# Performance work log

Hardware: AMD Instinct MI355X
Metric: run time of the kernel (lower is better)

Reference implementation:

```python
import jax, jax.numpy as jnp
import numpy as np

B, U, N, D, O = 64, 8, 2048, 512, 512  # batch, units, neurons, input_dim, output_dim
RES_CONN, IN_CONN, BIAS_P = 0.2, 0.2, 0.5


def setup_inputs() -> dict:
    key = jax.random.key(0)
    ks = jax.random.split(key, 10)
    # Recurrent weights: normal * sparse mask, normalized by ~spectral radius
    Wd = jax.random.normal(ks[0], (U, N, N), dtype=jnp.float32)
    Wmask = (jax.random.uniform(ks[1], (U, N, N)) < RES_CONN).astype(jnp.float32)
    W = Wd * Wmask / jnp.sqrt(RES_CONN * N)  # approx unit spectral radius
    # Input weights: fixed_bernoulli -> {0,1} sparse matrix
    Win = (jax.random.uniform(ks[2], (U, D, N)) < IN_CONN).astype(jnp.float32)
    bias = (jax.random.uniform(ks[3], (U, 1, N)) < BIAS_P).astype(jnp.float32)
    Wout = jax.random.normal(ks[4], (U, N, O), dtype=jnp.float32)
    sr = jax.random.uniform(ks[5], (U, 1, 1), dtype=jnp.float32)
    adaptive_lr = jax.random.uniform(ks[6], (U, D, 1), dtype=jnp.float32)
    temperature = jnp.ones((1,), dtype=jnp.float32)
    X = jax.random.normal(ks[7], (B, U, D), dtype=jnp.float32)
    state = jax.random.normal(ks[8], (B, U, N), dtype=jnp.float32)
    return {"X": X, "state": state, "W": W, "Win": Win, "bias": bias,
            "Wout": Wout, "sr": sr, "adaptive_lr": adaptive_lr,
            "temperature": temperature}


def reference(X, state, W, Win, bias, Wout, sr, adaptive_lr, temperature):
    # X: [B,U,D], state: [B,U,N]
    x = X[:, :, None, :]       # [B,U,1,D]
    s = state[:, :, None, :]   # [B,U,1,N]
    # adaptive learning rate: softmax over units
    logits = jnp.einsum('buid,udk->buik', x, adaptive_lr) / temperature  # [B,U,1,1]
    lr = jax.nn.softmax(logits, axis=1)
    # _sparse_mm_subhead == masked matmul (W's zeros contribute nothing)
    feed = jnp.einsum('bud,udn->bun', X, Win)[:, :, None, :]           # [B,U,1,N]
    echo = jnp.einsum('bun,unm->bum', state, W * sr)[:, :, None, :] + bias
    new_state = (1.0 - lr) * s + lr * jnp.tanh(feed + echo)            # [B,U,1,N]
    output = jnp.einsum('buin,uno->buio', new_state, Wout)             # [B,U,1,O]
    return new_state.squeeze(2), output.squeeze(2)
```

## Files before the change

### kernel.cpp

```cpp
#include <hip/hip_runtime.h>

#define B_ 64
#define U_ 8
#define N_ 2048
#define D_ 512
#define O_ 512
#define NS_ELEMS ((long)B_ * U_ * N_)
#define OUT_ELEMS ((long)B_ * U_ * O_)

typedef __attribute__((ext_vector_type(8))) short short8;
typedef __attribute__((ext_vector_type(8))) float float8;
typedef __attribute__((ext_vector_type(4))) float float4v;
typedef __attribute__((ext_vector_type(4))) unsigned short ushort4v;
typedef __attribute__((ext_vector_type(16))) float floatx16;

__device__ __forceinline__ float bf2f(unsigned short b) {
    unsigned int u = ((unsigned int)b) << 16;
    float f; __builtin_memcpy(&f, &u, 4); return f;
}
__device__ __forceinline__ unsigned short f2bf(float f) {
    unsigned int u; __builtin_memcpy(&u, &f, 4);
    u += 0x7FFFu + ((u >> 16) & 1u);
    return (unsigned short)(u >> 16);
}
__device__ __forceinline__ bool is_bf(const void* temp) {
    return ((const unsigned short*)temp)[0] == 0x3F80u;
}
__device__ __forceinline__ float ldg1(const void* p, long i, bool bf) {
    return bf ? bf2f(((const unsigned short*)p)[i]) : ((const float*)p)[i];
}
__device__ __forceinline__ short8 ld8(const void* p, long i, bool bf) {
    if (bf) return *(const short8*)((const unsigned short*)p + i);
    float8 v = *(const float8*)((const float*)p + i);
    short8 r;
#pragma unroll
    for (int e = 0; e < 8; ++e) r[e] = (short)f2bf(v[e]);
    return r;
}
__device__ __forceinline__ short8 ld8s(const void* p, long i, bool bf, float s) {
    short8 r;
    if (bf) {
        short8 v = *(const short8*)((const unsigned short*)p + i);
#pragma unroll
        for (int e = 0; e < 8; ++e) r[e] = (short)f2bf(bf2f((unsigned short)v[e]) * s);
    } else {
        float8 v = *(const float8*)((const float*)p + i);
#pragma unroll
        for (int e = 0; e < 8; ++e) r[e] = (short)f2bf(v[e] * s);
    }
    return r;
}
__device__ __forceinline__ void stg1(void* p, long i, bool bf, float v) {
    if (bf) ((unsigned short*)p)[i] = f2bf(v); else ((float*)p)[i] = v;
}
__device__ __forceinline__ int swz(int row, int kbyte) {
    return row * 128 + (kbyte ^ ((row & 7) << 4));
}

__device__ __forceinline__ void gl_lds16(const void* g, void* l) {
    __builtin_amdgcn_global_load_lds(
        (const __attribute__((address_space(1))) unsigned int*)g,
        (__attribute__((address_space(3))) unsigned int*)l, 16, 0, 0);
}
#define WAITV(n) asm volatile("s_waitcnt vmcnt(" #n ")" ::: "memory")

template<bool BF, int NCH>
__device__ __forceinline__ void gemm_wide(
        const char* __restrict__ Apan, long arow_b,
        const char* __restrict__ Bpan, long brow_b,
        char* __restrict__ As,
        char* __restrict__ Bs,
        floatx16& acc0, floatx16& acc1, int t) {
    const int w = t >> 6, l = t & 63;
    const int mrow = (w >> 1) * 32 + (l & 31);
    const int nc0 = (w & 1) * 64 + (l & 31);
    const int BCH = BF ? 16384 : 32768;
    const int a_r = w * 16 + (l >> 3);
    const long a_g = 16 * ((l & 7) ^ (l >> 3));

#define ISSUE2(ck)                                                                  \
    {   char* Ad = As + ((ck) & 1) * 8192 + w * 2048;                               \
        const char* Ag0 = Apan + (long)(ck) * 128;                                  \
        gl_lds16(Ag0 + (long)a_r * arow_b + a_g, Ad);                               \
        gl_lds16(Ag0 + (long)(a_r + 8) * arow_b + a_g, Ad + 1024);                  \
        char* Bd = Bs + ((ck) & 1) * BCH;                                           \
        if (BF) {                                                                   \
            _Pragma("unroll")                                                       \
            for (int i = 0; i < 4; ++i) {                                           \
                int kr = (ck) * 64 + w * 16 + i * 4 + (l >> 4);                     \
                gl_lds16(Bpan + (long)kr * brow_b + (l & 15) * 16,                  \
                         Bd + (w * 16 + i * 4) * 256);                              \
            }                                                                       \
        } else {                                                                    \
            _Pragma("unroll")                                                       \
            for (int i = 0; i < 8; ++i) {                                           \
                int kr = (ck) * 64 + w * 16 + i * 2 + (l >> 5);                     \
                gl_lds16(Bpan + (long)kr * brow_b + (l & 31) * 16,                  \
                         Bd + (w * 16 + i * 2) * 512);                              \
            }                                                                       \
        } }

    ISSUE2(0);
#pragma unroll
    for (int ck = 0; ck < NCH; ++ck) {
        if (ck + 1 < NCH) ISSUE2(ck + 1);
        __builtin_amdgcn_sched_barrier(0);
        if (ck + 1 < NCH) { if (BF) { WAITV(6); } else { WAITV(10); } }
        else { WAITV(0); }
        __builtin_amdgcn_s_barrier();
        __builtin_amdgcn_sched_barrier(0);
        const char* Ac = As + (ck & 1) * 8192;
        const char* Bc = Bs + (ck & 1) * BCH;
#pragma unroll
        for (int ks = 0; ks < 4; ++ks) {
            int g = 2 * ks + (l >> 5);
            short8 a = *(const short8*)(Ac + swz(mrow, g * 16));
            short8 b0, b1;
            if (BF) {
#pragma unroll
                for (int e = 0; e < 8; ++e) {
                    b0[e] = *(const short*)(Bc + (g * 8 + e) * 256 + nc0 * 2);
                    b1[e] = *(const short*)(Bc + (g * 8 + e) * 256 + (nc0 + 32) * 2);
                }
            } else {
#pragma unroll
                for (int e = 0; e < 8; ++e) {
                    b0[e] = (short)f2bf(*(const float*)(Bc + (g * 8 + e) * 512 + nc0 * 4));
                    b1[e] = (short)f2bf(*(const float*)(Bc + (g * 8 + e) * 512 + (nc0 + 32) * 4));
                }
            }
            acc0 = __builtin_amdgcn_mfma_f32_32x32x16_bf16(a, b0, acc0, 0, 0, 0);
            acc1 = __builtin_amdgcn_mfma_f32_32x32x16_bf16(a, b1, acc1, 0, 0, 0);
        }
        __builtin_amdgcn_sched_barrier(0);
        __builtin_amdgcn_s_barrier();
    }
#undef ISSUE2
}

__global__ __launch_bounds__(256) void k01(
        const void* __restrict__ state, const void* __restrict__ X,
        const void* __restrict__ sr, const void* __restrict__ alr,
        const void* __restrict__ temp,
        unsigned short* __restrict__ stC, unsigned short* __restrict__ xC,
        float* __restrict__ lrbuf) {
    const bool bf = is_bf(temp);
    const int bid = blockIdx.x;
    const int t = threadIdx.x;
    __shared__ float lg[U_];
    if (bid < 1280) {
        const long i = ((long)bid * 256 + t) * 4;
        ushort4v o;
        if (i < NS_ELEMS) {
            const int u = (int)(i >> 17);
            const float srv = ldg1(sr, u, bf);
#pragma unroll
            for (int e = 0; e < 4; ++e) {
                const long j = i + e;
                const int b = (int)((j >> 11) & 63), k = (int)(j & 2047);
                o[e] = f2bf(ldg1(state, (long)(b * 8 + u) * 2048 + k, bf) * srv);
            }
            *(ushort4v*)(stC + i) = o;
        } else {
            const long j0 = i - NS_ELEMS;
            const int u = (int)(j0 >> 15);
#pragma unroll
            for (int e = 0; e < 4; ++e) {
                const long j = j0 + e;
                const int b = (int)((j >> 9) & 63), k = (int)(j & 511);
                o[e] = f2bf(ldg1(X, (long)(b * 8 + u) * 512 + k, bf));
            }
            *(ushort4v*)(xC + j0) = o;
        }
    } else {
        const int b = bid - 1280;
        const int u = t >> 5, ln = t & 31;
        float s = 0.f;
#pragma unroll
        for (int j = 0; j < 16; ++j) {
            int d = ln * 16 + j;
            s += ldg1(X, (long)(b * 8 + u) * 512 + d, bf) * ldg1(alr, u * 512 + d, bf);
        }
#pragma unroll
        for (int off = 1; off < 32; off <<= 1) s += __shfl_xor(s, off);
        const float T = ldg1(temp, 0, bf);
        if (ln == 0) lg[u] = s / T;
        __syncthreads();
        if (t < U_) {
            float m = lg[0];
#pragma unroll
            for (int i = 1; i < U_; ++i) m = fmaxf(m, lg[i]);
            float den = 0.f;
#pragma unroll
            for (int i = 0; i < U_; ++i) den += expf(lg[i] - m);
            lrbuf[b * U_ + t] = expf(lg[t] - m) / den;
        }
    }
}

template<bool BF>
__device__ __forceinline__ void k2w_body(
        const unsigned short* stC, const unsigned short* xC,
        const void* W, const void* Win, unsigned short* slabs,
        char* As, char* Bs, int bid, int t) {
    const int seg = bid >> 7;
    const int u   = (bid >> 4) & 7;
    const int nb  = bid & 15;
    const int n0  = nb * 128;
    const int w = t >> 6, l = t & 63;
    const long esz = BF ? 2 : 4;
    floatx16 acc0, acc1;
#pragma unroll
    for (int i = 0; i < 16; ++i) { acc0[i] = 0.f; acc1[i] = 0.f; }

    const char* stP = (const char*)stC + (long)u * 262144;
    const char* Wp  = (const char*)W + ((long)u * N_ * N_ + n0) * esz;

    if (seg == 0) {
        gemm_wide<BF, 8>((const char*)xC + (long)u * 65536, 1024,
                         (const char*)Win + ((long)u * D_ * N_ + n0) * esz, N_ * esz,
                         As, Bs, acc0, acc1, t);
        gemm_wide<BF, 2>(stP, 4096, Wp, N_ * esz, As, Bs, acc0, acc1, t);
    } else if (seg == 1) {
        gemm_wide<BF, 10>(stP + 256, 4096, Wp + (long)128 * N_ * esz, N_ * esz,
                          As, Bs, acc0, acc1, t);
    } else if (seg == 2) {
        gemm_wide<BF, 10>(stP + 1536, 4096, Wp + (long)768 * N_ * esz, N_ * esz,
                          As, Bs, acc0, acc1, t);
    } else {
        gemm_wide<BF, 10>(stP + 2816, 4096, Wp + (long)1408 * N_ * esz, N_ * esz,
                          As, Bs, acc0, acc1, t);
    }
    unsigned short* slab = slabs + (long)seg * NS_ELEMS;
    const int n = n0 + (w & 1) * 64 + (l & 31);
    const int rowbase = (w >> 1) * 32 + 4 * (l >> 5);
#pragma unroll
    for (int r = 0; r < 16; ++r) {
        int b = rowbase + (r & 3) + 8 * (r >> 2);
        slab[(long)b * (U_ * N_) + u * N_ + n] = f2bf(acc0[r]);
        slab[(long)b * (U_ * N_) + u * N_ + n + 32] = f2bf(acc1[r]);
    }
}

__global__ __launch_bounds__(256) void k2_wide(
        const unsigned short* __restrict__ stC, const unsigned short* __restrict__ xC,
        const void* __restrict__ W, const void* __restrict__ Win,
        const void* __restrict__ temp, unsigned short* __restrict__ slabs) {
    __shared__ alignas(16) char As[2 * 8192];
    __shared__ alignas(16) char Bs[2 * 32768];
    const int bid = (blockIdx.x % 8) * 64 + blockIdx.x / 8;
    if (is_bf(temp))
        k2w_body<true >(stC, xC, W, Win, slabs, As, Bs, bid, threadIdx.x);
    else
        k2w_body<false>(stC, xC, W, Win, slabs, As, Bs, bid, threadIdx.x);
}

__global__ void k2b_mix(const unsigned short* __restrict__ slabs,
                        const void* __restrict__ state,
                        const void* __restrict__ bias, const void* __restrict__ temp,
                        const float* __restrict__ lrbuf, void* __restrict__ ns,
                        unsigned short* __restrict__ nsC) {
    const bool bf = is_bf(temp);
    const long i = ((long)blockIdx.x * 256 + threadIdx.x) * 4;
    const int b = (int)(i >> 14);
    const int un = (int)(i & 16383);
    const int u = un >> 11, n = un & 2047;
    float4v s;
    {
        ushort4v v0 = *(const ushort4v*)(slabs + i);
        ushort4v v1 = *(const ushort4v*)(slabs + NS_ELEMS + i);
        ushort4v v2 = *(const ushort4v*)(slabs + 2 * NS_ELEMS + i);
        ushort4v v3 = *(const ushort4v*)(slabs + 3 * NS_ELEMS + i);
#pragma unroll
        for (int e = 0; e < 4; ++e)
            s[e] = (bf2f(v0[e]) + bf2f(v1[e])) + (bf2f(v2[e]) + bf2f(v3[e]));
    }
    const float lr = lrbuf[b * U_ + u];
    ushort4v oc;
#pragma unroll
    for (int e = 0; e < 4; ++e) {
        float st = ldg1(state, i + e, bf);
        float bv = ldg1(bias, u * N_ + n + e, bf);
        float v = (1.f - lr) * st + lr * tanhf(s[e] + bv);
        stg1(ns, i + e, bf, v);
        oc[e] = f2bf(v);
    }
    *(ushort4v*)(nsC + ((long)u * 64 + b) * 2048 + n) = oc;
}

template<bool BF>
__device__ __forceinline__ void k3w_body(
        const unsigned short* nsC, const void* Wout, unsigned short* part,
        char* As, char* Bs, int bid, int t) {
    const int kc = bid >> 5;
    const int u  = (bid >> 2) & 7;
    const int ot = bid & 3;
    const int o0 = ot * 128;
    const int w = t >> 6, l = t & 63;
    const long esz = BF ? 2 : 4;
    floatx16 acc0, acc1;
#pragma unroll
    for (int i = 0; i < 16; ++i) { acc0[i] = 0.f; acc1[i] = 0.f; }
    gemm_wide<BF, 4>((const char*)nsC + (long)u * 262144 + (long)kc * 512, 4096,
                     (const char*)Wout + ((long)u * N_ * O_ + (long)kc * 256 * O_ + o0) * esz,
                     O_ * esz, As, Bs, acc0, acc1, t);
    unsigned short* slab = part + (long)((kc * 8 + u) * 4 + ot) * 8192;
    const int oo = (w & 1) * 64 + (l & 31);
    const int rowbase = (w >> 1) * 32 + 4 * (l >> 5);
#pragma unroll
    for (int r = 0; r < 16; ++r) {
        int b = rowbase + (r & 3) + 8 * (r >> 2);
        slab[b * 128 + oo] = f2bf(acc0[r]);
        slab[b * 128 + oo + 32] = f2bf(acc1[r]);
    }
}

__global__ __launch_bounds__(256) void k3_wide(
        const unsigned short* __restrict__ nsC, const void* __restrict__ Wout,
        const void* __restrict__ temp, unsigned short* __restrict__ part) {
    __shared__ alignas(16) char As[2 * 8192];
    __shared__ alignas(16) char Bs[2 * 32768];
    const int bid = (blockIdx.x % 8) * 32 + blockIdx.x / 8;
    if (is_bf(temp))
        k3w_body<true >(nsC, Wout, part, As, Bs, bid, threadIdx.x);
    else
        k3w_body<false>(nsC, Wout, part, As, Bs, bid, threadIdx.x);
}

__global__ void k3_reduce(const unsigned short* __restrict__ part,
                          const void* __restrict__ temp,
                          void* __restrict__ outfull) {
    const bool bf = is_bf(temp);
    int i = blockIdx.x * 256 + threadIdx.x;
    int b = i >> 12;
    int u = (i >> 9) & 7;
    int o = i & 511;
    int ot = o >> 7, oo = o & 127;
    float s = 0.f;
#pragma unroll
    for (int kc = 0; kc < 8; ++kc)
        s += bf2f(part[(long)((kc * 8 + u) * 4 + ot) * 8192 + b * 128 + oo]);
    stg1(outfull, NS_ELEMS + i, bf, s);
}

__global__ __launch_bounds__(256) void k2_state(
        const void* __restrict__ X, const void* __restrict__ state,
        const void* __restrict__ W, const void* __restrict__ Win,
        const void* __restrict__ bias, const void* __restrict__ sr,
        const void* __restrict__ temp, const float* __restrict__ lrbuf,
        void* __restrict__ ns) {
    const bool bf = is_bf(temp);
    const int u  = blockIdx.x >> 5;
    const int n0 = (blockIdx.x & 31) * 64;
    const int t = threadIdx.x;
    const int w = t >> 6, l = t & 63;
    __shared__ alignas(16) char As[8192];
    __shared__ alignas(16) char Bs[8192];
    const float srv = ldg1(sr, u, bf);
    floatx16 acc;
#pragma unroll
    for (int i = 0; i < 16; ++i) acc[i] = 0.f;
    for (int ck = 0; ck < 40; ++ck) {
        const bool feed = ck < 8;
        const void* Ag; long aoff; int lda; float ascale;
        const void* Bg; long boff;
        if (feed) {
            Ag = X;   aoff = (long)u * D_ + ck * 64;          lda = U_ * D_; ascale = 1.f;
            Bg = Win; boff = (long)u * D_ * N_ + (long)(ck * 64) * N_ + n0;
        } else {
            Ag = state; aoff = (long)u * N_ + (ck - 8) * 64;  lda = U_ * N_; ascale = srv;
            Bg = W;     boff = (long)u * N_ * N_ + (long)((ck - 8) * 64) * N_ + n0;
        }
        __syncthreads();
#pragma unroll
        for (int j = 0; j < 2; ++j) {
            int idx = j * 256 + t;
            int row = idx >> 3, cch = idx & 7;
            short8 v = ld8s(Ag, aoff + (long)row * lda + cch * 8, bf, ascale);
            *(short8*)(As + swz(row, cch * 16)) = v;
        }
#pragma unroll
        for (int j = 0; j < 2; ++j) {
            int k = t & 63;
            int c = (t >> 6) + 4 * j;
            short8 v = ld8(Bg, boff + (long)k * N_ + c * 8, bf);
#pragma unroll
            for (int e = 0; e < 8; ++e) {
                int n = c * 8 + e;
                *(unsigned short*)(Bs + swz(n, 2 * k)) = (unsigned short)v[e];
            }
        }
        __syncthreads();
        const int mrow = (w >> 1) * 32 + (l & 31);
        const int ncol = (w & 1) * 32 + (l & 31);
#pragma unroll
        for (int ks = 0; ks < 4; ++ks) {
            int g = 2 * ks + (l >> 5);
            short8 a = *(const short8*)(As + swz(mrow, g * 16));
            short8 b = *(const short8*)(Bs + swz(ncol, g * 16));
            acc = __builtin_amdgcn_mfma_f32_32x32x16_bf16(a, b, acc, 0, 0, 0);
        }
    }
    const int n = n0 + (w & 1) * 32 + (l & 31);
    const int rowbase = (w >> 1) * 32 + 4 * (l >> 5);
    const float biasv = ldg1(bias, u * N_ + n, bf);
#pragma unroll
    for (int r = 0; r < 16; ++r) {
        int b = rowbase + (r & 3) + 8 * (r >> 2);
        float lr = lrbuf[b * U_ + u];
        float st = ldg1(state, (long)b * U_ * N_ + u * N_ + n, bf);
        float v = (1.f - lr) * st + lr * tanhf(acc[r] + biasv);
        stg1(ns, (long)b * U_ * N_ + u * N_ + n, bf, v);
    }
}

__global__ __launch_bounds__(256) void k3_mono(
        const void* __restrict__ ns, const void* __restrict__ Wout,
        const void* __restrict__ temp, void* __restrict__ outfull) {
    const bool bf = is_bf(temp);
    const int u  = (blockIdx.x >> 3) & 7;
    const int ot = blockIdx.x & 7;
    const int o0 = ot * 64;
    const int t = threadIdx.x;
    const int w = t >> 6, l = t & 63;
    __shared__ alignas(16) char As[8192];
    __shared__ alignas(16) char Bs[8192];
    floatx16 acc;
#pragma unroll
    for (int i = 0; i < 16; ++i) acc[i] = 0.f;
    for (int ck = 0; ck < 32; ++ck) {
        const long ka = (long)(ck * 64);
        __syncthreads();
#pragma unroll
        for (int j = 0; j < 2; ++j) {
            int idx = j * 256 + t;
            int row = idx >> 3, cch = idx & 7;
            short8 v = ld8(ns, (long)row * (U_ * N_) + u * N_ + ka + cch * 8, bf);
            *(short8*)(As + swz(row, cch * 16)) = v;
        }
#pragma unroll
        for (int j = 0; j < 2; ++j) {
            int k = t & 63;
            int c = (t >> 6) + 4 * j;
            short8 v = ld8(Wout, (long)u * N_ * O_ + (ka + k) * O_ + o0 + c * 8, bf);
#pragma unroll
            for (int e = 0; e < 8; ++e) {
                int n = c * 8 + e;
                *(unsigned short*)(Bs + swz(n, 2 * k)) = (unsigned short)v[e];
            }
        }
        __syncthreads();
        const int mrow = (w >> 1) * 32 + (l & 31);
        const int ncol = (w & 1) * 32 + (l & 31);
#pragma unroll
        for (int ks = 0; ks < 4; ++ks) {
            int g = 2 * ks + (l >> 5);
            short8 a = *(const short8*)(As + swz(mrow, g * 16));
            short8 b = *(const short8*)(Bs + swz(ncol, g * 16));
            acc = __builtin_amdgcn_mfma_f32_32x32x16_bf16(a, b, acc, 0, 0, 0);
        }
    }
    const int oo = (w & 1) * 32 + (l & 31);
    const int rowbase = (w >> 1) * 32 + 4 * (l >> 5);
#pragma unroll
    for (int r = 0; r < 16; ++r) {
        int b = rowbase + (r & 3) + 8 * (r >> 2);
        stg1(outfull, NS_ELEMS + (long)b * U_ * O_ + u * O_ + o0 + oo, bf, acc[r]);
    }
}

extern "C" void kernel_launch(void* const* d_in, const int* in_sizes, int n_in,
                              void* d_out, int out_size, void* d_ws, size_t ws_size,
                              hipStream_t stream) {
    const void* X     = d_in[0];
    const void* state = d_in[1];
    const void* W     = d_in[2];
    const void* Win   = d_in[3];
    const void* bias  = d_in[4];
    const void* Wout  = d_in[5];
    const void* sr    = d_in[6];
    const void* alr   = d_in[7];
    const void* temp  = d_in[8];

    char* base = (char*)d_ws;
    float* lrbuf        = (float*)base;
    unsigned short* stC = (unsigned short*)(base + 4096);
    unsigned short* xC  = (unsigned short*)(base + 4096 + (2u << 20));
    unsigned short* nsC = (unsigned short*)(base + 4096 + (2u << 20) + (512u << 10));
    unsigned short* slabs = (unsigned short*)(base + (8u << 20));
    const size_t need = (8u << 20) + 4 * (size_t)NS_ELEMS * 2;

    if (ws_size >= need) {
        k01      <<<1344, 256, 0, stream>>>(state, X, sr, alr, temp, stC, xC, lrbuf);
        k2_wide  <<<512, 256, 0, stream>>>(stC, xC, W, Win, temp, slabs);
        k2b_mix  <<<NS_ELEMS / 1024, 256, 0, stream>>>(slabs, state, bias, temp, lrbuf, d_out, nsC);
        k3_wide  <<<256, 256, 0, stream>>>(nsC, Wout, temp, slabs);
        k3_reduce<<<OUT_ELEMS / 256, 256, 0, stream>>>(slabs, temp, d_out);
    } else {
        k01      <<<1344, 256, 0, stream>>>(state, X, sr, alr, temp,
                                            (unsigned short*)base, (unsigned short*)base, lrbuf);
        k2_state <<<256, 256, 0, stream>>>(X, state, W, Win, bias, sr, temp, lrbuf, d_out);
        k3_mono  <<<64, 256, 0, stream>>>(d_out, Wout, temp, d_out);
    }
}
```

Before: 59.48 us.

## Widen recurrent GEMM tile to 256 columns with 2x2 MFMA per wave

Replaces the 128-column GEMM tile in the state/input kernel with a 256-column tile. Each wave now covers all 64 batch rows across 64 columns using four 32x32 MFMA accumulators. Grid size halves to 256 blocks, so each A-panel load is reused over twice as many columns. In exchange the B staging buffer doubles (up to 128KB of LDS in fp32 mode), which lowers occupancy, and the grid drops to one block per CU or fewer.

Measured after the change: 61.86 us. 1.04x slower.

```diff
diff --git a/kernel.cpp b/kernel.cpp
--- a/kernel.cpp
+++ b/kernel.cpp
@@ -63,6 +63,83 @@
         (__attribute__((address_space(3))) unsigned int*)l, 16, 0, 0);
 }
 #define WAITV(n) asm volatile("s_waitcnt vmcnt(" #n ")" ::: "memory")
+
+template<bool BF, int NCH>
+__device__ __forceinline__ void gemm_w256(
+        const char* __restrict__ Apan, long arow_b,
+        const char* __restrict__ Bpan, long brow_b,
+        char* __restrict__ As,
+        char* __restrict__ Bs,
+        floatx16& a00, floatx16& a01, floatx16& a10, floatx16& a11, int t) {
+    const int w = t >> 6, l = t & 63;
+    const int BCH = BF ? 32768 : 65536;
+    const int BROW = BF ? 512 : 1024;
+    const int a_r = w * 16 + (l >> 3);
+    const long a_g = 16 * ((l & 7) ^ (l >> 3));
+
+#define ISSUE3(ck)                                                                  \
+    {   char* Ad = As + ((ck) & 1) * 8192 + w * 2048;                               \
+        const char* Ag0 = Apan + (long)(ck) * 128;                                  \
+        gl_lds16(Ag0 + (long)a_r * arow_b + a_g, Ad);                               \
+        gl_lds16(Ag0 + (long)(a_r + 8) * arow_b + a_g, Ad + 1024);                  \
+        char* Bd = Bs + ((ck) & 1) * BCH;                                           \
+        if (BF) {                                                                   \
+            _Pragma("unroll")                                                       \
+            for (int i = 0; i < 8; ++i) {                                           \
+                int kr = (ck) * 64 + w * 16 + i * 2 + (l >> 5);                     \
+                gl_lds16(Bpan + (long)kr * brow_b + (l & 31) * 16,                  \
+                         Bd + (w * 16 + i * 2) * 512);                              \
+            }                                                                       \
+        } else {                                                                    \
+            _Pragma("unroll")                                                       \
+            for (int i = 0; i < 16; ++i) {                                          \
+                int kr = (ck) * 64 + w * 16 + i;                                    \
+                gl_lds16(Bpan + (long)kr * brow_b + (long)l * 16,                   \
+                         Bd + (w * 16 + i) * 1024);                                 \
+            }                                                                       \
+        } }
+
+    ISSUE3(0);
+#pragma unroll
+    for (int ck = 0; ck < NCH; ++ck) {
+        if (ck + 1 < NCH) ISSUE3(ck + 1);
+        __builtin_amdgcn_sched_barrier(0);
+        if (ck + 1 < NCH) { if (BF) { WAITV(10); } else { WAITV(18); } }
+        else { WAITV(0); }
+        __builtin_amdgcn_s_barrier();
+        __builtin_amdgcn_sched_barrier(0);
+        const char* Ac = As + (ck & 1) * 8192;
+        const char* Bc = Bs + (ck & 1) * BCH;
+        const int c0 = w * 64 + (l & 31);
+#pragma unroll
+        for (int ks = 0; ks < 4; ++ks) {
+            int g = 2 * ks + (l >> 5);
+            short8 ar0 = *(const short8*)(Ac + swz(l & 31, g * 16));
+            short8 ar1 = *(const short8*)(Ac + swz((l & 31) + 32, g * 16));
+            short8 b0, b1;
+            if (BF) {
+#pragma unroll
+                for (int e = 0; e < 8; ++e) {
+                    b0[e] = *(const short*)(Bc + (g * 8 + e) * 512 + c0 * 2);
+                    b1[e] = *(const short*)(Bc + (g * 8 + e) * 512 + (c0 + 32) * 2);
+                }
+            } else {
+#pragma unroll
+                for (int e = 0; e < 8; ++e) {
+                    b0[e] = (short)f2bf(*(const float*)(Bc + (g * 8 + e) * 1024 + c0 * 4));
+                    b1[e] = (short)f2bf(*(const float*)(Bc + (g * 8 + e) * 1024 + (c0 + 32) * 4));
+                }
+            }
+            a00 = __builtin_amdgcn_mfma_f32_32x32x16_bf16(ar0, b0, a00, 0, 0, 0);
+            a01 = __builtin_amdgcn_mfma_f32_32x32x16_bf16(ar0, b1, a01, 0, 0, 0);
+            a10 = __builtin_amdgcn_mfma_f32_32x32x16_bf16(ar1, b0, a10, 0, 0, 0);
+            a11 = __builtin_amdgcn_mfma_f32_32x32x16_bf16(ar1, b1, a11, 0, 0, 0);
+        }
+        __builtin_amdgcn_sched_barrier(0);
+        __builtin_amdgcn_s_barrier();
+    }
+#undef ISSUE3
+}
 
 template<bool BF, int NCH>
 __device__ __forceinline__ void gemm_wide(
@@ -203,42 +280,44 @@
         const unsigned short* stC, const unsigned short* xC,
         const void* W, const void* Win, unsigned short* slabs,
         char* As, char* Bs, int bid, int t) {
-    const int seg = bid >> 7;
-    const int u   = (bid >> 4) & 7;
-    const int nb  = bid & 15;
-    const int n0  = nb * 128;
+    const int seg = bid >> 6;
+    const int u   = (bid >> 3) & 7;
+    const int nb  = bid & 7;
+    const int n0  = nb * 256;
     const int w = t >> 6, l = t & 63;
     const long esz = BF ? 2 : 4;
-    floatx16 acc0, acc1;
-#pragma unroll
-    for (int i = 0; i < 16; ++i) { acc0[i] = 0.f; acc1[i] = 0.f; }
+    floatx16 a00, a01, a10, a11;
+#pragma unroll
+    for (int i = 0; i < 16; ++i) { a00[i] = 0.f; a01[i] = 0.f; a10[i] = 0.f; a11[i] = 0.f; }
 
     const char* stP = (const char*)stC + (long)u * 262144;
     const char* Wp  = (const char*)W + ((long)u * N_ * N_ + n0) * esz;
 
     if (seg == 0) {
-        gemm_wide<BF, 8>((const char*)xC + (long)u * 65536, 1024,
+        gemm_w256<BF, 8>((const char*)xC + (long)u * 65536, 1024,
                          (const char*)Win + ((long)u * D_ * N_ + n0) * esz, N_ * esz,
-                         As, Bs, acc0, acc1, t);
-        gemm_wide<BF, 2>(stP, 4096, Wp, N_ * esz, As, Bs, acc0, acc1, t);
+                         As, Bs, a00, a01, a10, a11, t);
+        gemm_w256<BF, 2>(stP, 4096, Wp, N_ * esz, As, Bs, a00, a01, a10, a11, t);
     } else if (seg == 1) {
-        gemm_wide<BF, 10>(stP + 256, 4096, Wp + (long)128 * N_ * esz, N_ * esz,
-                          As, Bs, acc0, acc1, t);
+        gemm_w256<BF, 10>(stP + 256, 4096, Wp + (long)128 * N_ * esz, N_ * esz,
+                          As, Bs, a00, a01, a10, a11, t);
     } else if (seg == 2) {
-        gemm_wide<BF, 10>(stP + 1536, 4096, Wp + (long)768 * N_ * esz, N_ * esz,
-                          As, Bs, acc0, acc1, t);
+        gemm_w256<BF, 10>(stP + 1536, 4096, Wp + (long)768 * N_ * esz, N_ * esz,
+                          As, Bs, a00, a01, a10, a11, t);
     } else {
-        gemm_wide<BF, 10>(stP + 2816, 4096, Wp + (long)1408 * N_ * esz, N_ * esz,
-                          As, Bs, acc0, acc1, t);
+        gemm_w256<BF, 10>(stP + 2816, 4096, Wp + (long)1408 * N_ * esz, N_ * esz,
+                          As, Bs, a00, a01, a10, a11, t);
     }
     unsigned short* slab = slabs + (long)seg * NS_ELEMS;
-    const int n = n0 + (w & 1) * 64 + (l & 31);
-    const int rowbase = (w >> 1) * 32 + 4 * (l >> 5);
+    const int n = n0 + w * 64 + (l & 31);
+    const int rowbase = 4 * (l >> 5);
 #pragma unroll
     for (int r = 0; r < 16; ++r) {
         int b = rowbase + (r & 3) + 8 * (r >> 2);
-        slab[(long)b * (U_ * N_) + u * N_ + n] = f2bf(acc0[r]);
-        slab[(long)b * (U_ * N_) + u * N_ + n + 32] = f2bf(acc1[r]);
+        slab[(long)b * (U_ * N_) + u * N_ + n]            = f2bf(a00[r]);
+        slab[(long)b * (U_ * N_) + u * N_ + n + 32]       = f2bf(a01[r]);
+        slab[(long)(b + 32) * (U_ * N_) + u * N_ + n]     = f2bf(a10[r]);
+        slab[(long)(b + 32) * (U_ * N_) + u * N_ + n + 32] = f2bf(a11[r]);
     }
 }
 
@@ -247,8 +326,8 @@
         const void* __restrict__ W, const void* __restrict__ Win,
         const void* __restrict__ temp, unsigned short* __restrict__ slabs) {
     __shared__ alignas(16) char As[2 * 8192];
-    __shared__ alignas(16) char Bs[2 * 32768];
-    const int bid = (blockIdx.x % 8) * 64 + blockIdx.x / 8;
+    __shared__ alignas(16) char Bs[2 * 65536];
+    const int bid = (blockIdx.x % 8) * 32 + blockIdx.x / 8;
     if (is_bf(temp))
         k2w_body<true >(stC, xC, W, Win, slabs, As, Bs, bid, threadIdx.x);
     else
@@ -492,7 +571,7 @@
 
     if (ws_size >= need) {
         k01      <<<1344, 256, 0, stream>>>(state, X, sr, alr, temp, stC, xC, lrbuf);
-        k2_wide  <<<512, 256, 0, stream>>>(stC, xC, W, Win, temp, slabs);
+        k2_wide  <<<256, 256, 0, stream>>>(stC, xC, W, Win, temp, slabs);
         k2b_mix  <<<NS_ELEMS / 1024, 256, 0, stream>>>(slabs, state, bias, temp, lrbuf, d_out, nsC);
         k3_wide  <<<256, 256, 0, stream>>>(nsC, Wout, temp, slabs);
         k3_reduce<<<OUT_ELEMS / 256, 256, 0, stream>>>(slabs, temp, d_out);
```
